# Kernel optimization log

Measured on AMD Instinct MI355X. Metric: run time of the kernel, lower is better.

Reference implementation:

```python
import jax, jax.numpy as jnp
import numpy as np

N = 50000
E = 600000
D = 128
EPS = 1e-5  # nn.LayerNorm default eps


def gcn_conv(x, W, b, src, dst):
    # PyG GCNConv with add_self_loops=True, edge_weight=None (all ones),
    # symmetric normalization D^-1/2 (A+I) D^-1/2.
    h = x @ W                                        # [N, D]
    deg = jnp.zeros((N,), h.dtype).at[dst].add(1.0) + 1.0  # +1 for self loop
    dinv = jax.lax.rsqrt(deg)                        # deg >= 1, safe
    norm = dinv[src] * dinv[dst]                     # [E]
    msg = h[src] * norm[:, None]                     # [E, D] gather
    agg = jax.ops.segment_sum(msg, dst, num_segments=N)
    agg = agg + h * (dinv * dinv)[:, None]           # self-loop term
    return agg + b


def layer_norm(x, g, b):
    mu = jnp.mean(x, axis=-1, keepdims=True)
    var = jnp.mean(jnp.square(x - mu), axis=-1, keepdims=True)
    return (x - mu) * jax.lax.rsqrt(var + EPS) * g + b


def setup_inputs() -> dict:
    key = jax.random.key(0)
    ks = jax.random.split(key, 6)
    x = jax.random.normal(ks[0], (N, D), dtype=jnp.float32)
    edge_index = jax.random.randint(ks[1], (2, E), 0, N, dtype=jnp.int64)
    s = 1.0 / np.sqrt(D)
    W1 = jax.random.uniform(ks[2], (D, D), jnp.float32, -s, s)
    W2 = jax.random.uniform(ks[3], (D, D), jnp.float32, -s, s)
    b1 = jnp.zeros((D,), jnp.float32)
    b2 = jnp.zeros((D,), jnp.float32)
    ln1_g = jnp.ones((D,), jnp.float32)
    ln1_b = jnp.zeros((D,), jnp.float32)
    ln2_g = jnp.ones((D,), jnp.float32)
    ln2_b = jnp.zeros((D,), jnp.float32)
    return {"x": x, "edge_index": edge_index, "W1": W1, "b1": b1,
            "ln1_g": ln1_g, "ln1_b": ln1_b, "W2": W2, "b2": b2,
            "ln2_g": ln2_g, "ln2_b": ln2_b}


def reference(x, edge_index, W1, b1, ln1_g, ln1_b, W2, b2, ln2_g, ln2_b):
    src, dst = edge_index[0], edge_index[1]
    out = gcn_conv(x, W1, b1, src, dst)
    out = jax.nn.relu(layer_norm(out, ln1_g, ln1_b))  # dropout = identity (eval)
    out = gcn_conv(out, W2, b2, src, dst)
    out = jax.nn.relu(layer_norm(out, ln2_g, ln2_b))
    return out + x
```

## Files before the change

kernel.cpp:

```cpp
#include <hip/hip_runtime.h>
#include <hip/hip_fp16.h>

#define D 128
#define EPS 1e-5f
#define KB 64
#define NBSH 7
#define BUCKW 128

typedef unsigned int u32;
typedef unsigned short u16;
typedef unsigned char u8;
typedef __attribute__((ext_vector_type(8))) _Float16 half8;
typedef __attribute__((ext_vector_type(4))) float f32x4;
typedef __attribute__((ext_vector_type(2))) float f32x2;

__device__ inline u16 f2h(float x) {
  _Float16 t = (_Float16)x;
  return __builtin_bit_cast(u16, t);
}
__device__ inline u8 f2fp8(float x) {
  return (u8)(__builtin_amdgcn_cvt_pk_fp8_f32(x, x, 0, false) & 0xff);
}

__global__ __launch_bounds__(256) void k_prep(const float* __restrict__ W1,
                                              const float* __restrict__ W2,
                                              u16* __restrict__ Wt1,
                                              u16* __restrict__ Wt2) {
  int i = blockIdx.x * 256 + threadIdx.x;
  if (i < 2 * D * D) {
    const float* W = (i < D * D) ? W1 : W2;
    u16* Wt = (i < D * D) ? Wt1 : Wt2;
    int ii = i & (D * D - 1);
    int k = ii >> 7, c = ii & 127;
    Wt[c * D + k] = f2h(W[ii]);
  }
}

template <bool F32IN>
__device__ __forceinline__ void gemm_body(const void* __restrict__ in_,
                                          const u16* __restrict__ Wt,
                                          u8* __restrict__ out, int nrows,
                                          int blk) {
  const int tid = threadIdx.x;
  const int lane = tid & 63, wv = tid >> 6;
  const int m = lane & 15, q = lane >> 4;
  const int r0 = blk * 64 + wv * 16;
  const int rowa = min(r0 + m, nrows - 1);

  f32x4 acc[8];
#pragma unroll
  for (int ct = 0; ct < 8; ct++) acc[ct] = (f32x4)(0.0f);

#pragma unroll
  for (int kk = 0; kk < 4; kk++) {
    const int kbase = kk * 32 + q * 8;
    half8 a;
    if (F32IN) {
      const float* in = (const float*)in_;
      float4 v0 = *(const float4*)(in + (size_t)rowa * D + kbase);
      float4 v1 = *(const float4*)(in + (size_t)rowa * D + kbase + 4);
      a[0] = (_Float16)v0.x; a[1] = (_Float16)v0.y;
      a[2] = (_Float16)v0.z; a[3] = (_Float16)v0.w;
      a[4] = (_Float16)v1.x; a[5] = (_Float16)v1.y;
      a[6] = (_Float16)v1.z; a[7] = (_Float16)v1.w;
    } else {
      const u16* in = (const u16*)in_;
      a = *(const half8*)(in + (size_t)rowa * D + kbase);
    }
#pragma unroll
    for (int ct = 0; ct < 8; ct++) {
      half8 b = *(const half8*)(Wt + (ct * 16 + m) * D + kbase);
      acc[ct] = __builtin_amdgcn_mfma_f32_16x16x32_f16(a, b, acc[ct], 0, 0, 0);
    }
  }

#pragma unroll
  for (int ct = 0; ct < 8; ct++) {
#pragma unroll
    for (int rg = 0; rg < 4; rg++) {
      int rr = r0 + q * 4 + rg;
      if (rr < nrows) out[(size_t)rr * D + ct * 16 + m] = f2fp8(acc[ct][rg]);
    }
  }
}

__global__ __launch_bounds__(256) void k_count_gemm1(
    const int* __restrict__ dst, int* __restrict__ cnt, int E, int NB, int EPB,
    const float* __restrict__ x, const u16* __restrict__ Wt1,
    u8* __restrict__ A, int nrows) {
  if (blockIdx.x < (u32)KB) {
    __shared__ int hist[512];
    const int k = blockIdx.x, tid = threadIdx.x;
    for (int i = tid; i < NB; i += 256) hist[i] = 0;
    __syncthreads();
    const int e0 = k * EPB, e1 = min(E, e0 + EPB);
    for (int base = e0 + tid; base < e1; base += 2048) {
      int dd[8];
#pragma unroll
      for (int i = 0; i < 8; i++) {
        int e = base + i * 256;
        dd[i] = (e < e1) ? dst[e] : -1;
      }
#pragma unroll
      for (int i = 0; i < 8; i++)
        if (dd[i] >= 0) atomicAdd(&hist[dd[i] >> NBSH], 1);
    }
    __syncthreads();
    for (int b = tid; b < NB; b += 256) cnt[b * KB + k] = hist[b];
  } else {
    gemm_body<true>(x, Wt1, A, nrows, blockIdx.x - KB);
  }
}

__global__ __launch_bounds__(1024) void k_scan(int* __restrict__ cnt, int M,
                                               int NB, int* __restrict__ bsv,
                                               int E) {
  __shared__ int wt[16];
  const int tid = threadIdx.x;
  const int lane = tid & 63, wid = tid >> 6;
  const int chunks = (M + 1023) >> 10;
  int running = 0;
  int i = tid;
  int v = (i < M) ? cnt[i] : 0;
  for (int c = 0; c < chunks; c++) {
    int inext = i + 1024;
    int vnext = (c + 1 < chunks && inext < M) ? cnt[inext] : 0;
    int incl = v;
#pragma unroll
    for (int o = 1; o < 64; o <<= 1) {
      int t = __shfl_up(incl, o, 64);
      if (lane >= o) incl += t;
    }
    if (lane == 63) wt[wid] = incl;
    __syncthreads();
    int woff = 0, total = 0;
#pragma unroll
    for (int j = 0; j < 16; j++) {
      int t = wt[j];
      if (j < wid) woff += t;
      total += t;
    }
    int excl = running + woff + incl - v;
    if (i < M) {
      cnt[i] = excl;
      if ((i & (KB - 1)) == 0) bsv[i / KB] = excl;
    }
    running += total;
    __syncthreads();
    i = inext;
    v = vnext;
  }
  if (tid == 0) bsv[NB] = E;
}

__global__ __launch_bounds__(256) void k_scatter(
    const int* __restrict__ src, const int* __restrict__ dst,
    const int* __restrict__ cnt, u32* __restrict__ tmp, int E, int NB,
    int EPB) {
  __shared__ int off[512];
  const int k = blockIdx.x, tid = threadIdx.x;
  for (int b = tid; b < NB; b += 256) off[b] = cnt[b * KB + k];
  __syncthreads();
  const int e0 = k * EPB, e1 = min(E, e0 + EPB);
  for (int base = e0 + tid; base < e1; base += 2048) {
    int dd[8], ss[8];
#pragma unroll
    for (int i = 0; i < 8; i++) {
      int e = base + i * 256;
      dd[i] = (e < e1) ? dst[e] : -1;
      ss[i] = (e < e1) ? src[e] : 0;
    }
#pragma unroll
    for (int i = 0; i < 8; i++) {
      if (dd[i] >= 0) {
        int p = atomicAdd(&off[dd[i] >> NBSH], 1);
        tmp[p] = (u32)ss[i] | ((u32)(dd[i] & (BUCKW - 1)) << 16);
      }
    }
  }
}

__global__ __launch_bounds__(256) void k_bucket(
    const u32* __restrict__ tmp, const int* __restrict__ bsv,
    int4* __restrict__ meta, float* __restrict__ dinv,
    u32* __restrict__ csr, int N) {
  __shared__ int hist[BUCKW];
  __shared__ int sc[BUCKW];
  __shared__ int cur[BUCKW];
  const int b = blockIdx.x, tid = threadIdx.x;
  const int s0 = bsv[b], s1 = bsv[b + 1];
  if (tid < BUCKW) hist[tid] = 0;
  __syncthreads();
  for (int base = s0 + tid; base < s1; base += 1024) {
    int tt[4];
#pragma unroll
    for (int i = 0; i < 4; i++) {
      int idx = base + i * 256;
      tt[i] = (idx < s1) ? (int)tmp[idx] : -1;
    }
#pragma unroll
    for (int i = 0; i < 4; i++)
      if (tt[i] >= 0) atomicAdd(&hist[(tt[i] >> 16) & (BUCKW - 1)], 1);
  }
  __syncthreads();
  if (tid < BUCKW) sc[tid] = hist[tid];
  __syncthreads();
#pragma unroll
  for (int o = 1; o < BUCKW; o <<= 1) {
    int t = 0;
    if (tid < BUCKW && tid >= o) t = sc[tid - o];
    __syncthreads();
    if (tid < BUCKW) sc[tid] += t;
    __syncthreads();
  }
  if (tid < BUCKW) {
    int dg = hist[tid];
    int excl = sc[tid] - dg;
    cur[tid] = excl;
    int d = (b << NBSH) + tid;
    if (d < N) {
      float dv = rsqrtf((float)dg + 1.0f);
      meta[d] = make_int4(s0 + excl, dg, __builtin_bit_cast(int, dv), 0);
      dinv[d] = dv;
    }
  }
  __syncthreads();
  for (int base = s0 + tid; base < s1; base += 1024) {
    int tt[4];
#pragma unroll
    for (int i = 0; i < 4; i++) {
      int idx = base + i * 256;
      tt[i] = (idx < s1) ? (int)tmp[idx] : -1;
    }
#pragma unroll
    for (int i = 0; i < 4; i++) {
      if (tt[i] >= 0) {
        int r = atomicAdd(&cur[(tt[i] >> 16) & (BUCKW - 1)], 1);
        csr[s0 + r] = (u32)tt[i] & 0xffffu;
      }
    }
  }
}

__global__ __launch_bounds__(256) void k_weights(
    const int4* __restrict__ meta, const float* __restrict__ dinv,
    u32* __restrict__ csr, int N) {
  int gid = blockIdx.x * 256 + threadIdx.x;
  int r = gid >> 2, j0 = gid & 3;
  if (r >= N) return;
  int4 mt = meta[r];
  float dv = __builtin_bit_cast(float, mt.z);
  for (int j = j0; j < mt.y; j += 4) {
    u32 s = csr[mt.x + j];
    float w = dinv[s] * dv;
    csr[mt.x + j] = s | ((u32)f2h(w) << 16);
  }
}

#define ACC_EDGE(vv, ee)                                                     \
  {                                                                          \
    float ww = (float)__builtin_bit_cast(_Float16, (u16)((ee) >> 16));       \
    f32x2 p_;                                                                \
    p_ = __builtin_amdgcn_cvt_pk_f32_fp8(vv.x, false);                       \
    acc[0] = fmaf(p_[0], ww, acc[0]); acc[1] = fmaf(p_[1], ww, acc[1]);      \
    p_ = __builtin_amdgcn_cvt_pk_f32_fp8(vv.x, true);                        \
    acc[2] = fmaf(p_[0], ww, acc[2]); acc[3] = fmaf(p_[1], ww, acc[3]);      \
    p_ = __builtin_amdgcn_cvt_pk_f32_fp8(vv.y, false);                       \
    acc[4] = fmaf(p_[0], ww, acc[4]); acc[5] = fmaf(p_[1], ww, acc[5]);      \
    p_ = __builtin_amdgcn_cvt_pk_f32_fp8(vv.y, true);                        \
    acc[6] = fmaf(p_[0], ww, acc[6]); acc[7] = fmaf(p_[1], ww, acc[7]);      \
  }

__device__ __forceinline__ void gather_ln_core(
    const uint2* __restrict__ hb, const int4* __restrict__ meta,
    const u32* __restrict__ csr, const float* __restrict__ b,
    const float* __restrict__ g, const float* __restrict__ bln,
    int row, int n, int sl, float out[8]) {
  const bool valid = row < n;
  const int rc = valid ? row : 0;
  int4 mt = meta[rc];
  int beg = mt.x;
  int cnt = valid ? mt.y : 0;
  float dv = __builtin_bit_cast(float, mt.z);
  float sn = dv * dv;

  float acc[8];
  {
    uint2 su = hb[(size_t)rc * 16 + sl];
    f32x2 p0 = __builtin_amdgcn_cvt_pk_f32_fp8(su.x, false);
    f32x2 p1 = __builtin_amdgcn_cvt_pk_f32_fp8(su.x, true);
    f32x2 p2 = __builtin_amdgcn_cvt_pk_f32_fp8(su.y, false);
    f32x2 p3 = __builtin_amdgcn_cvt_pk_f32_fp8(su.y, true);
    acc[0] = p0[0] * sn; acc[1] = p0[1] * sn;
    acc[2] = p1[0] * sn; acc[3] = p1[1] * sn;
    acc[4] = p2[0] * sn; acc[5] = p2[1] * sn;
    acc[6] = p3[0] * sn; acc[7] = p3[1] * sn;
  }

  int cm = max(cnt, __shfl_xor(cnt, 16, 64));
  cm = max(cm, __shfl_xor(cm, 32, 64));

  u32 epre = 0u;
  if (sl < cnt) epre = csr[beg + sl];

  for (int j0 = 0; j0 < cm; j0 += 16) {
    u32 ecur = epre;
    epre = 0u;
    {
      int nj = j0 + 16;
      if (nj < cm && sl < cnt - nj) epre = csr[beg + nj + sl];
    }
    int mm = min(cm - j0, 16);
    for (int j = 0; j < mm; j += 8) {
      u32 e0 = __shfl(ecur, j + 0, 16), e1 = __shfl(ecur, j + 1, 16);
      u32 e2 = __shfl(ecur, j + 2, 16), e3 = __shfl(ecur, j + 3, 16);
      u32 e4 = __shfl(ecur, j + 4, 16), e5 = __shfl(ecur, j + 5, 16);
      u32 e6 = __shfl(ecur, j + 6, 16), e7 = __shfl(ecur, j + 7, 16);
      uint2 v0 = hb[(size_t)(e0 & 0xffffu) * 16 + sl];
      uint2 v1 = hb[(size_t)(e1 & 0xffffu) * 16 + sl];
      uint2 v2 = hb[(size_t)(e2 & 0xffffu) * 16 + sl];
      uint2 v3 = hb[(size_t)(e3 & 0xffffu) * 16 + sl];
      uint2 v4 = hb[(size_t)(e4 & 0xffffu) * 16 + sl];
      uint2 v5 = hb[(size_t)(e5 & 0xffffu) * 16 + sl];
      uint2 v6 = hb[(size_t)(e6 & 0xffffu) * 16 + sl];
      uint2 v7 = hb[(size_t)(e7 & 0xffffu) * 16 + sl];
      ACC_EDGE(v0, e0);
      ACC_EDGE(v1, e1);
      ACC_EDGE(v2, e2);
      ACC_EDGE(v3, e3);
      ACC_EDGE(v4, e4);
      ACC_EDGE(v5, e5);
      ACC_EDGE(v6, e6);
      ACC_EDGE(v7, e7);
    }
  }

  int d0 = sl * 8;
  float4 bb0 = *(const float4*)(b + d0);
  float4 bb1 = *(const float4*)(b + d0 + 4);
  float a0 = acc[0] + bb0.x, a1 = acc[1] + bb0.y;
  float a2 = acc[2] + bb0.z, a3 = acc[3] + bb0.w;
  float a4 = acc[4] + bb1.x, a5 = acc[5] + bb1.y;
  float a6 = acc[6] + bb1.z, a7 = acc[7] + bb1.w;

  float sum = ((a0 + a1) + (a2 + a3)) + ((a4 + a5) + (a6 + a7));
#pragma unroll
  for (int o = 8; o >= 1; o >>= 1) sum += __shfl_xor(sum, o, 16);
  float mu = sum * (1.0f / 128.0f);
  float e0 = a0 - mu, e1 = a1 - mu, e2 = a2 - mu, e3 = a3 - mu;
  float e4 = a4 - mu, e5 = a5 - mu, e6 = a6 - mu, e7 = a7 - mu;
  float vs = ((e0 * e0 + e1 * e1) + (e2 * e2 + e3 * e3)) +
             ((e4 * e4 + e5 * e5) + (e6 * e6 + e7 * e7));
#pragma unroll
  for (int o = 8; o >= 1; o >>= 1) vs += __shfl_xor(vs, o, 16);
  float inv = rsqrtf(vs * (1.0f / 128.0f) + EPS);

  float4 gg0 = *(const float4*)(g + d0);
  float4 gg1 = *(const float4*)(g + d0 + 4);
  float4 bl0 = *(const float4*)(bln + d0);
  float4 bl1 = *(const float4*)(bln + d0 + 4);
  out[0] = fmaxf(e0 * inv * gg0.x + bl0.x, 0.0f);
  out[1] = fmaxf(e1 * inv * gg0.y + bl0.y, 0.0f);
  out[2] = fmaxf(e2 * inv * gg0.z + bl0.z, 0.0f);
  out[3] = fmaxf(e3 * inv * gg0.w + bl0.w, 0.0f);
  out[4] = fmaxf(e4 * inv * gg1.x + bl1.x, 0.0f);
  out[5] = fmaxf(e5 * inv * gg1.y + bl1.y, 0.0f);
  out[6] = fmaxf(e6 * inv * gg1.z + bl1.z, 0.0f);
  out[7] = fmaxf(e7 * inv * gg1.w + bl1.w, 0.0f);
}

__global__ __launch_bounds__(256, 8) void k_gather1(
    const uint2* __restrict__ hb, const int4* __restrict__ meta,
    const u32* __restrict__ csr,
    const float* __restrict__ b, const float* __restrict__ g,
    const float* __restrict__ bln,
    u16* __restrict__ y1, int n) {
  const int tid = threadIdx.x;
  const int sl = tid & 15;
  const int row = blockIdx.x * 16 + (tid >> 4);
  float o[8];
  gather_ln_core(hb, meta, csr, b, g, bln, row, n, sl, o);
  if (row >= n) return;
  uint4 pk;
  pk.x = ((u32)f2h(o[1]) << 16) | (u32)f2h(o[0]);
  pk.y = ((u32)f2h(o[3]) << 16) | (u32)f2h(o[2]);
  pk.z = ((u32)f2h(o[5]) << 16) | (u32)f2h(o[4]);
  pk.w = ((u32)f2h(o[7]) << 16) | (u32)f2h(o[6]);
  *(uint4*)(y1 + (size_t)row * D + sl * 8) = pk;
}

__global__ __launch_bounds__(256) void k_gemm2(const u16* __restrict__ y1,
                                               const u16* __restrict__ Wt2,
                                               u8* __restrict__ outB, int n) {
  gemm_body<false>(y1, Wt2, outB, n, blockIdx.x);
}

__global__ __launch_bounds__(256, 8) void k_gather2(
    const uint2* __restrict__ hb, const int4* __restrict__ meta,
    const u32* __restrict__ csr,
    const float* __restrict__ b, const float* __restrict__ g,
    const float* __restrict__ bln, const float* __restrict__ resid,
    float* __restrict__ outf, int n) {
  const int tid = threadIdx.x;
  const int sl = tid & 15;
  const int row = blockIdx.x * 16 + (tid >> 4);
  float o[8];
  gather_ln_core(hb, meta, csr, b, g, bln, row, n, sl, o);
  if (row >= n) return;
  size_t base = (size_t)row * D + sl * 8;
  float4 r0 = *(const float4*)(resid + base);
  float4 r1 = *(const float4*)(resid + base + 4);
  *(float4*)(outf + base) =
      make_float4(o[0] + r0.x, o[1] + r0.y, o[2] + r0.z, o[3] + r0.w);
  *(float4*)(outf + base + 4) =
      make_float4(o[4] + r1.x, o[5] + r1.y, o[6] + r1.z, o[7] + r1.w);
}

extern "C" void kernel_launch(void* const* d_in, const int* in_sizes, int n_in,
                              void* d_out, int out_size, void* d_ws, size_t ws_size,
                              hipStream_t stream) {
  const float* x    = (const float*)d_in[0];
  const int*   ei   = (const int*)d_in[1];
  const float* W1   = (const float*)d_in[2];
  const float* b1   = (const float*)d_in[3];
  const float* g1   = (const float*)d_in[4];
  const float* bl1  = (const float*)d_in[5];
  const float* W2   = (const float*)d_in[6];
  const float* b2   = (const float*)d_in[7];
  const float* g2   = (const float*)d_in[8];
  const float* bl2  = (const float*)d_in[9];

  const int N = in_sizes[0] / D;
  const int E = in_sizes[1] / 2;
  const int* src = ei;
  const int* dst = ei + E;

  const int NB  = (N + BUCKW - 1) / BUCKW;
  const int M   = NB * KB;
  const int EPB = (E + KB - 1) / KB;
  const int GB  = (N + 63) / 64;
  const int RB  = (N + 15) / 16;

  size_t off = 0;
  auto walloc = [&](size_t bytes) {
    void* p = (char*)d_ws + off;
    off = (off + bytes + 255) & ~(size_t)255;
    return p;
  };
  int*   cnt   = (int*)walloc((size_t)M * 4);
  int*   bsv   = (int*)walloc((size_t)(NB + 1) * 4);
  u32*   tmp   = (u32*)walloc((size_t)E * 4);
  u32*   csr   = (u32*)walloc((size_t)E * 4);
  int4*  meta  = (int4*)walloc((size_t)N * 16);
  float* dinv  = (float*)walloc((size_t)N * 4);
  u8*    A     = (u8*)walloc((size_t)N * D);
  u8*    B     = (u8*)walloc((size_t)N * D);
  u16*   Wt1   = (u16*)walloc((size_t)D * D * 2);
  u16*   Wt2   = (u16*)walloc((size_t)D * D * 2);
  u16*   y1    = (u16*)walloc((size_t)N * D * 2);
  float* O     = (float*)d_out;

  k_prep<<<(2 * D * D + 255) / 256, 256, 0, stream>>>(W1, W2, Wt1, Wt2);
  k_count_gemm1<<<KB + GB, 256, 0, stream>>>(dst, cnt, E, NB, EPB, x, Wt1, A, N);
  k_scan<<<1, 1024, 0, stream>>>(cnt, M, NB, bsv, E);
  k_scatter<<<KB, 256, 0, stream>>>(src, dst, cnt, tmp, E, NB, EPB);
  k_bucket<<<NB, 256, 0, stream>>>(tmp, bsv, meta, dinv, csr, N);
  k_weights<<<(N * 4 + 255) / 256, 256, 0, stream>>>(meta, dinv, csr, N);
  k_gather1<<<RB, 256, 0, stream>>>((const uint2*)A, meta, csr, b1, g1, bl1,
                                    y1, N);
  k_gemm2<<<GB, 256, 0, stream>>>(y1, Wt2, B, N);
  k_gather2<<<RB, 256, 0, stream>>>((const uint2*)B, meta, csr,
                                    b2, g2, bl2, x, O, N);
}
```

Before: 207.8 us.

## Build CSR via global per-node degree atomics instead of bucketed two-level sort

Replaces the bucketed counting sort (per-block histograms, scan, scatter, per-bucket local sort, separate weight pass) with per-node global atomic degree counts, a single scan over N nodes that also writes meta and dinv, and one scatter that places edges with their normalization weights already packed. This removes three kernel launches and the temporary edge buffer. It relies on global atomics to contended addresses and a single-block scan over 50k entries. The CSR order within a row becomes nondeterministic, which can change fp summation order. The gather loop also drops the shuffle-based prefetch of edge indices and loads them directly per lane instead.

```diff
diff --git a/kernel.cpp b/kernel.cpp
--- a/kernel.cpp
+++ b/kernel.cpp
@@ -3,9 +3,7 @@
 
 #define D 128
 #define EPS 1e-5f
-#define KB 64
-#define NBSH 7
-#define BUCKW 128
+#define CB 128
 
 typedef unsigned int u32;
 typedef unsigned short u16;
@@ -25,14 +23,18 @@
 __global__ __launch_bounds__(256) void k_prep(const float* __restrict__ W1,
                                               const float* __restrict__ W2,
                                               u16* __restrict__ Wt1,
-                                              u16* __restrict__ Wt2) {
-  int i = blockIdx.x * 256 + threadIdx.x;
-  if (i < 2 * D * D) {
+                                              u16* __restrict__ Wt2,
+                                              int* __restrict__ deg, int N) {
+  if (blockIdx.x < 128) {
+    int i = blockIdx.x * 256 + threadIdx.x;
     const float* W = (i < D * D) ? W1 : W2;
     u16* Wt = (i < D * D) ? Wt1 : Wt2;
     int ii = i & (D * D - 1);
     int k = ii >> 7, c = ii & 127;
     Wt[c * D + k] = f2h(W[ii]);
+  } else {
+    int i = (blockIdx.x - 128) * 256 + threadIdx.x;
+    if (i < N) deg[i] = 0;
   }
 }
 
@@ -85,46 +87,43 @@
 }
 
 __global__ __launch_bounds__(256) void k_count_gemm1(
-    const int* __restrict__ dst, int* __restrict__ cnt, int E, int NB, int EPB,
+    const int* __restrict__ dst, int* __restrict__ deg, int E, int EPB,
     const float* __restrict__ x, const u16* __restrict__ Wt1,
     u8* __restrict__ A, int nrows) {
-  if (blockIdx.x < (u32)KB) {
-    __shared__ int hist[512];
+  if (blockIdx.x < (u32)CB) {
     const int k = blockIdx.x, tid = threadIdx.x;
-    for (int i = tid; i < NB; i += 256) hist[i] = 0;
-    __syncthreads();
     const int e0 = k * EPB, e1 = min(E, e0 + EPB);
-    for (int base = e0 + tid; base < e1; base += 2048) {
-      int dd[8];
-#pragma unroll
-      for (int i = 0; i < 8; i++) {
+    for (int base = e0 + tid; base < e1; base += 1024) {
+      int dd[4];
+#pragma unroll
+      for (int i = 0; i < 4; i++) {
         int e = base + i * 256;
         dd[i] = (e < e1) ? dst[e] : -1;
       }
 #pragma unroll
-      for (int i = 0; i < 8; i++)
-        if (dd[i] >= 0) atomicAdd(&hist[dd[i] >> NBSH], 1);
-    }
-    __syncthreads();
-    for (int b = tid; b < NB; b += 256) cnt[b * KB + k] = hist[b];
+      for (int i = 0; i < 4; i++)
+        if (dd[i] >= 0) atomicAdd(&deg[dd[i]], 1);
+    }
   } else {
-    gemm_body<true>(x, Wt1, A, nrows, blockIdx.x - KB);
-  }
-}
-
-__global__ __launch_bounds__(1024) void k_scan(int* __restrict__ cnt, int M,
-                                               int NB, int* __restrict__ bsv,
-                                               int E) {
+    gemm_body<true>(x, Wt1, A, nrows, blockIdx.x - CB);
+  }
+}
+
+__global__ __launch_bounds__(1024) void k_scan(const int* __restrict__ deg,
+                                               int4* __restrict__ meta,
+                                               float* __restrict__ dinv,
+                                               int* __restrict__ cursor,
+                                               int N) {
   __shared__ int wt[16];
   const int tid = threadIdx.x;
   const int lane = tid & 63, wid = tid >> 6;
-  const int chunks = (M + 1023) >> 10;
+  const int chunks = (N + 1023) >> 10;
   int running = 0;
   int i = tid;
-  int v = (i < M) ? cnt[i] : 0;
+  int v = (i < N) ? deg[i] : 0;
   for (int c = 0; c < chunks; c++) {
     int inext = i + 1024;
-    int vnext = (c + 1 < chunks && inext < M) ? cnt[inext] : 0;
+    int vnext = (c + 1 < chunks && inext < N) ? deg[inext] : 0;
     int incl = v;
 #pragma unroll
     for (int o = 1; o < 64; o <<= 1) {
@@ -141,119 +140,46 @@
       total += t;
     }
     int excl = running + woff + incl - v;
-    if (i < M) {
-      cnt[i] = excl;
-      if ((i & (KB - 1)) == 0) bsv[i / KB] = excl;
+    if (i < N) {
+      float dv = rsqrtf((float)v + 1.0f);
+      meta[i] = make_int4(excl, v, __builtin_bit_cast(int, dv), 0);
+      dinv[i] = dv;
+      cursor[i] = excl;
     }
     running += total;
     __syncthreads();
     i = inext;
     v = vnext;
   }
-  if (tid == 0) bsv[NB] = E;
-}
-
-__global__ __launch_bounds__(256) void k_scatter(
+}
+
+__global__ __launch_bounds__(256) void k_scatter2(
     const int* __restrict__ src, const int* __restrict__ dst,
-    const int* __restrict__ cnt, u32* __restrict__ tmp, int E, int NB,
-    int EPB) {
-  __shared__ int off[512];
-  const int k = blockIdx.x, tid = threadIdx.x;
-  for (int b = tid; b < NB; b += 256) off[b] = cnt[b * KB + k];
-  __syncthreads();
-  const int e0 = k * EPB, e1 = min(E, e0 + EPB);
-  for (int base = e0 + tid; base < e1; base += 2048) {
-    int dd[8], ss[8];
-#pragma unroll
-    for (int i = 0; i < 8; i++) {
-      int e = base + i * 256;
-      dd[i] = (e < e1) ? dst[e] : -1;
-      ss[i] = (e < e1) ? src[e] : 0;
-    }
-#pragma unroll
-    for (int i = 0; i < 8; i++) {
+    const float* __restrict__ dinv, int* __restrict__ cursor,
+    u32* __restrict__ csr, int E) {
+  const int stride = gridDim.x * 256;
+  int gid = blockIdx.x * 256 + threadIdx.x;
+  for (int base = gid; base < E; base += stride * 4) {
+    int ss[4], dd[4];
+#pragma unroll
+    for (int i = 0; i < 4; i++) {
+      int e = base + i * stride;
+      ss[i] = (e < E) ? src[e] : 0;
+      dd[i] = (e < E) ? dst[e] : -1;
+    }
+    float ws[4], wd[4];
+#pragma unroll
+    for (int i = 0; i < 4; i++) {
+      ws[i] = (dd[i] >= 0) ? dinv[ss[i]] : 0.0f;
+      wd[i] = (dd[i] >= 0) ? dinv[dd[i]] : 0.0f;
+    }
+#pragma unroll
+    for (int i = 0; i < 4; i++) {
       if (dd[i] >= 0) {
-        int p = atomicAdd(&off[dd[i] >> NBSH], 1);
-        tmp[p] = (u32)ss[i] | ((u32)(dd[i] & (BUCKW - 1)) << 16);
+        int p = atomicAdd(&cursor[dd[i]], 1);
+        csr[p] = (u32)ss[i] | ((u32)f2h(ws[i] * wd[i]) << 16);
       }
     }
-  }
-}
-
-__global__ __launch_bounds__(256) void k_bucket(
-    const u32* __restrict__ tmp, const int* __restrict__ bsv,
-    int4* __restrict__ meta, float* __restrict__ dinv,
-    u32* __restrict__ csr, int N) {
-  __shared__ int hist[BUCKW];
-  __shared__ int sc[BUCKW];
-  __shared__ int cur[BUCKW];
-  const int b = blockIdx.x, tid = threadIdx.x;
-  const int s0 = bsv[b], s1 = bsv[b + 1];
-  if (tid < BUCKW) hist[tid] = 0;
-  __syncthreads();
-  for (int base = s0 + tid; base < s1; base += 1024) {
-    int tt[4];
-#pragma unroll
-    for (int i = 0; i < 4; i++) {
-      int idx = base + i * 256;
-      tt[i] = (idx < s1) ? (int)tmp[idx] : -1;
-    }
-#pragma unroll
-    for (int i = 0; i < 4; i++)
-      if (tt[i] >= 0) atomicAdd(&hist[(tt[i] >> 16) & (BUCKW - 1)], 1);
-  }
-  __syncthreads();
-  if (tid < BUCKW) sc[tid] = hist[tid];
-  __syncthreads();
-#pragma unroll
-  for (int o = 1; o < BUCKW; o <<= 1) {
-    int t = 0;
-    if (tid < BUCKW && tid >= o) t = sc[tid - o];
-    __syncthreads();
-    if (tid < BUCKW) sc[tid] += t;
-    __syncthreads();
-  }
-  if (tid < BUCKW) {
-    int dg = hist[tid];
-    int excl = sc[tid] - dg;
-    cur[tid] = excl;
-    int d = (b << NBSH) + tid;
-    if (d < N) {
-      float dv = rsqrtf((float)dg + 1.0f);
-      meta[d] = make_int4(s0 + excl, dg, __builtin_bit_cast(int, dv), 0);
-      dinv[d] = dv;
-    }
-  }
-  __syncthreads();
-  for (int base = s0 + tid; base < s1; base += 1024) {
-    int tt[4];
-#pragma unroll
-    for (int i = 0; i < 4; i++) {
-      int idx = base + i * 256;
-      tt[i] = (idx < s1) ? (int)tmp[idx] : -1;
-    }
-#pragma unroll
-    for (int i = 0; i < 4; i++) {
-      if (tt[i] >= 0) {
-        int r = atomicAdd(&cur[(tt[i] >> 16) & (BUCKW - 1)], 1);
-        csr[s0 + r] = (u32)tt[i] & 0xffffu;
-      }
-    }
-  }
-}
-
-__global__ __launch_bounds__(256) void k_weights(
-    const int4* __restrict__ meta, const float* __restrict__ dinv,
-    u32* __restrict__ csr, int N) {
-  int gid = blockIdx.x * 256 + threadIdx.x;
-  int r = gid >> 2, j0 = gid & 3;
-  if (r >= N) return;
-  int4 mt = meta[r];
-  float dv = __builtin_bit_cast(float, mt.z);
-  for (int j = j0; j < mt.y; j += 4) {
-    u32 s = csr[mt.x + j];
-    float w = dinv[s] * dv;
-    csr[mt.x + j] = s | ((u32)f2h(w) << 16);
   }
 }
 
@@ -300,39 +226,19 @@
   int cm = max(cnt, __shfl_xor(cnt, 16, 64));
   cm = max(cm, __shfl_xor(cm, 32, 64));
 
-  u32 epre = 0u;
-  if (sl < cnt) epre = csr[beg + sl];
-
-  for (int j0 = 0; j0 < cm; j0 += 16) {
-    u32 ecur = epre;
-    epre = 0u;
-    {
-      int nj = j0 + 16;
-      if (nj < cm && sl < cnt - nj) epre = csr[beg + nj + sl];
-    }
-    int mm = min(cm - j0, 16);
-    for (int j = 0; j < mm; j += 8) {
-      u32 e0 = __shfl(ecur, j + 0, 16), e1 = __shfl(ecur, j + 1, 16);
-      u32 e2 = __shfl(ecur, j + 2, 16), e3 = __shfl(ecur, j + 3, 16);
-      u32 e4 = __shfl(ecur, j + 4, 16), e5 = __shfl(ecur, j + 5, 16);
-      u32 e6 = __shfl(ecur, j + 6, 16), e7 = __shfl(ecur, j + 7, 16);
-      uint2 v0 = hb[(size_t)(e0 & 0xffffu) * 16 + sl];
-      uint2 v1 = hb[(size_t)(e1 & 0xffffu) * 16 + sl];
-      uint2 v2 = hb[(size_t)(e2 & 0xffffu) * 16 + sl];
-      uint2 v3 = hb[(size_t)(e3 & 0xffffu) * 16 + sl];
-      uint2 v4 = hb[(size_t)(e4 & 0xffffu) * 16 + sl];
-      uint2 v5 = hb[(size_t)(e5 & 0xffffu) * 16 + sl];
-      uint2 v6 = hb[(size_t)(e6 & 0xffffu) * 16 + sl];
-      uint2 v7 = hb[(size_t)(e7 & 0xffffu) * 16 + sl];
-      ACC_EDGE(v0, e0);
-      ACC_EDGE(v1, e1);
-      ACC_EDGE(v2, e2);
-      ACC_EDGE(v3, e3);
-      ACC_EDGE(v4, e4);
-      ACC_EDGE(v5, e5);
-      ACC_EDGE(v6, e6);
-      ACC_EDGE(v7, e7);
-    }
+  for (int j0 = 0; j0 < cm; j0 += 8) {
+    u32 e[8];
+#pragma unroll
+    for (int jj = 0; jj < 8; jj++) {
+      int j = j0 + jj;
+      e[jj] = (j < cnt) ? csr[beg + j] : 0u;
+    }
+    uint2 v[8];
+#pragma unroll
+    for (int jj = 0; jj < 8; jj++)
+      v[jj] = hb[(size_t)(e[jj] & 0xffffu) * 16 + sl];
+#pragma unroll
+    for (int jj = 0; jj < 8; jj++) ACC_EDGE(v[jj], e[jj]);
   }
 
   int d0 = sl * 8;
@@ -435,11 +341,10 @@
   const int* src = ei;
   const int* dst = ei + E;
 
-  const int NB  = (N + BUCKW - 1) / BUCKW;
-  const int M   = NB * KB;
-  const int EPB = (E + KB - 1) / KB;
+  const int EPB = (E + CB - 1) / CB;
   const int GB  = (N + 63) / 64;
   const int RB  = (N + 15) / 16;
+  const int ZB  = (N + 255) / 256;
 
   size_t off = 0;
   auto walloc = [&](size_t bytes) {
@@ -447,10 +352,9 @@
     off = (off + bytes + 255) & ~(size_t)255;
     return p;
   };
-  int*   cnt   = (int*)walloc((size_t)M * 4);
-  int*   bsv   = (int*)walloc((size_t)(NB + 1) * 4);
-  u32*   tmp   = (u32*)walloc((size_t)E * 4);
-  u32*   csr   = (u32*)walloc((size_t)E * 4);
+  int*   deg   = (int*)walloc((size_t)N * 4);
+  int*   cursor= (int*)walloc((size_t)N * 4);
+  u32*   csr   = (u32*)walloc((size_t)E * 4 + 256);
   int4*  meta  = (int4*)walloc((size_t)N * 16);
   float* dinv  = (float*)walloc((size_t)N * 4);
   u8*    A     = (u8*)walloc((size_t)N * D);
@@ -460,12 +364,10 @@
   u16*   y1    = (u16*)walloc((size_t)N * D * 2);
   float* O     = (float*)d_out;
 
-  k_prep<<<(2 * D * D + 255) / 256, 256, 0, stream>>>(W1, W2, Wt1, Wt2);
-  k_count_gemm1<<<KB + GB, 256, 0, stream>>>(dst, cnt, E, NB, EPB, x, Wt1, A, N);
-  k_scan<<<1, 1024, 0, stream>>>(cnt, M, NB, bsv, E);
-  k_scatter<<<KB, 256, 0, stream>>>(src, dst, cnt, tmp, E, NB, EPB);
-  k_bucket<<<NB, 256, 0, stream>>>(tmp, bsv, meta, dinv, csr, N);
-  k_weights<<<(N * 4 + 255) / 256, 256, 0, stream>>>(meta, dinv, csr, N);
+  k_prep<<<128 + ZB, 256, 0, stream>>>(W1, W2, Wt1, Wt2, deg, N);
+  k_count_gemm1<<<CB + GB, 256, 0, stream>>>(dst, deg, E, EPB, x, Wt1, A, N);
+  k_scan<<<1, 1024, 0, stream>>>(deg, meta, dinv, cursor, N);
+  k_scatter2<<<512, 256, 0, stream>>>(src, dst, dinv, cursor, csr, E);
   k_gather1<<<RB, 256, 0, stream>>>((const uint2*)A, meta, csr, b1, g1, bl1,
                                     y1, N);
   k_gemm2<<<GB, 256, 0, stream>>>(y1, Wt2, B, N);
```

Result: slower. 272.1 us (+30.9%).

## Parallelize prefix scan across blocks and simplify gather edge-loading loop

Applied to the files above, without the earlier changes.

Replaces the single-block 1024-thread scan over the bucket count matrix with a three-kernel reduce/mid-scan/apply scheme that spreads the work over many blocks. The scan over M=NB*64 (~25k) entries was serialized in one workgroup. Separately, the gather loop drops the shuffle-based prefetch of CSR entries and instead has each lane load 8 CSR entries directly (broadcast loads) before issuing 8 feature gathers. This adds two extra kernel launches and loses the explicit next-chunk prefetch.

```diff
diff --git a/kernel.cpp b/kernel.cpp
--- a/kernel.cpp
+++ b/kernel.cpp
@@ -112,45 +112,86 @@
   }
 }
 
-__global__ __launch_bounds__(1024) void k_scan(int* __restrict__ cnt, int M,
-                                               int NB, int* __restrict__ bsv,
-                                               int E) {
-  __shared__ int wt[16];
-  const int tid = threadIdx.x;
-  const int lane = tid & 63, wid = tid >> 6;
-  const int chunks = (M + 1023) >> 10;
+__global__ __launch_bounds__(256) void k_scan_reduce(
+    const int* __restrict__ cnt, int M, int* __restrict__ bsum) {
+  const int b = blockIdx.x, t = threadIdx.x;
+  const int lane = t & 63, w = t >> 6;
+  int idx = b * 1024 + t * 4;
+  int4 v = make_int4(0, 0, 0, 0);
+  if (idx + 3 < M) {
+    v = *(const int4*)(cnt + idx);
+  } else {
+    if (idx + 0 < M) v.x = cnt[idx + 0];
+    if (idx + 1 < M) v.y = cnt[idx + 1];
+    if (idx + 2 < M) v.z = cnt[idx + 2];
+  }
+  int s = v.x + v.y + v.z + v.w;
+#pragma unroll
+  for (int o = 1; o < 64; o <<= 1) s += __shfl_xor(s, o, 64);
+  __shared__ int ws[4];
+  if (lane == 0) ws[w] = s;
+  __syncthreads();
+  if (t == 0) bsum[b] = ws[0] + ws[1] + ws[2] + ws[3];
+}
+
+__global__ __launch_bounds__(64) void k_scan_mid(const int* __restrict__ bsum,
+                                                 int* __restrict__ boff,
+                                                 int SB, int* __restrict__ bsv,
+                                                 int NB, int E) {
+  const int lane = threadIdx.x;
   int running = 0;
-  int i = tid;
-  int v = (i < M) ? cnt[i] : 0;
-  for (int c = 0; c < chunks; c++) {
-    int inext = i + 1024;
-    int vnext = (c + 1 < chunks && inext < M) ? cnt[inext] : 0;
+  for (int base = 0; base < SB; base += 64) {
+    int i = base + lane;
+    int v = (i < SB) ? bsum[i] : 0;
     int incl = v;
 #pragma unroll
     for (int o = 1; o < 64; o <<= 1) {
       int t = __shfl_up(incl, o, 64);
       if (lane >= o) incl += t;
     }
-    if (lane == 63) wt[wid] = incl;
-    __syncthreads();
-    int woff = 0, total = 0;
-#pragma unroll
-    for (int j = 0; j < 16; j++) {
-      int t = wt[j];
-      if (j < wid) woff += t;
-      total += t;
-    }
-    int excl = running + woff + incl - v;
-    if (i < M) {
-      cnt[i] = excl;
-      if ((i & (KB - 1)) == 0) bsv[i / KB] = excl;
-    }
-    running += total;
-    __syncthreads();
-    i = inext;
-    v = vnext;
-  }
-  if (tid == 0) bsv[NB] = E;
+    if (i < SB) boff[i] = running + incl - v;
+    running += __shfl(incl, 63, 64);
+  }
+  if (lane == 0) bsv[NB] = E;
+}
+
+__global__ __launch_bounds__(256) void k_scan_apply(
+    int* __restrict__ cnt, int M, const int* __restrict__ boff,
+    int* __restrict__ bsv) {
+  const int b = blockIdx.x, t = threadIdx.x;
+  const int lane = t & 63, w = t >> 6;
+  int idx = b * 1024 + t * 4;
+  int4 v = make_int4(0, 0, 0, 0);
+  if (idx + 3 < M) {
+    v = *(const int4*)(cnt + idx);
+  } else {
+    if (idx + 0 < M) v.x = cnt[idx + 0];
+    if (idx + 1 < M) v.y = cnt[idx + 1];
+    if (idx + 2 < M) v.z = cnt[idx + 2];
+  }
+  int s = v.x + v.y + v.z + v.w;
+  int incl = s;
+#pragma unroll
+  for (int o = 1; o < 64; o <<= 1) {
+    int u = __shfl_up(incl, o, 64);
+    if (lane >= o) incl += u;
+  }
+  __shared__ int ws[4];
+  if (lane == 63) ws[w] = incl;
+  __syncthreads();
+  int wbase = 0;
+#pragma unroll
+  for (int j = 0; j < 4; j++)
+    if (j < w) wbase += ws[j];
+  int base = boff[b] + wbase + incl - s;
+  int e0 = base, e1 = e0 + v.x, e2 = e1 + v.y, e3 = e2 + v.z;
+  if (idx < M) {
+    cnt[idx] = e0;
+    if ((idx & (KB - 1)) == 0) bsv[idx >> 6] = e0;
+  }
+  if (idx + 1 < M) cnt[idx + 1] = e1;
+  if (idx + 2 < M) cnt[idx + 2] = e2;
+  if (idx + 3 < M) cnt[idx + 3] = e3;
 }
 
 __global__ __launch_bounds__(256) void k_scatter(
@@ -300,39 +341,19 @@
   int cm = max(cnt, __shfl_xor(cnt, 16, 64));
   cm = max(cm, __shfl_xor(cm, 32, 64));
 
-  u32 epre = 0u;
-  if (sl < cnt) epre = csr[beg + sl];
-
-  for (int j0 = 0; j0 < cm; j0 += 16) {
-    u32 ecur = epre;
-    epre = 0u;
-    {
-      int nj = j0 + 16;
-      if (nj < cm && sl < cnt - nj) epre = csr[beg + nj + sl];
-    }
-    int mm = min(cm - j0, 16);
-    for (int j = 0; j < mm; j += 8) {
-      u32 e0 = __shfl(ecur, j + 0, 16), e1 = __shfl(ecur, j + 1, 16);
-      u32 e2 = __shfl(ecur, j + 2, 16), e3 = __shfl(ecur, j + 3, 16);
-      u32 e4 = __shfl(ecur, j + 4, 16), e5 = __shfl(ecur, j + 5, 16);
-      u32 e6 = __shfl(ecur, j + 6, 16), e7 = __shfl(ecur, j + 7, 16);
-      uint2 v0 = hb[(size_t)(e0 & 0xffffu) * 16 + sl];
-      uint2 v1 = hb[(size_t)(e1 & 0xffffu) * 16 + sl];
-      uint2 v2 = hb[(size_t)(e2 & 0xffffu) * 16 + sl];
-      uint2 v3 = hb[(size_t)(e3 & 0xffffu) * 16 + sl];
-      uint2 v4 = hb[(size_t)(e4 & 0xffffu) * 16 + sl];
-      uint2 v5 = hb[(size_t)(e5 & 0xffffu) * 16 + sl];
-      uint2 v6 = hb[(size_t)(e6 & 0xffffu) * 16 + sl];
-      uint2 v7 = hb[(size_t)(e7 & 0xffffu) * 16 + sl];
-      ACC_EDGE(v0, e0);
-      ACC_EDGE(v1, e1);
-      ACC_EDGE(v2, e2);
-      ACC_EDGE(v3, e3);
-      ACC_EDGE(v4, e4);
-      ACC_EDGE(v5, e5);
-      ACC_EDGE(v6, e6);
-      ACC_EDGE(v7, e7);
-    }
+  for (int j0 = 0; j0 < cm; j0 += 8) {
+    u32 e[8];
+#pragma unroll
+    for (int jj = 0; jj < 8; jj++) {
+      int j = j0 + jj;
+      e[jj] = (j < cnt) ? csr[beg + j] : 0u;
+    }
+    uint2 v[8];
+#pragma unroll
+    for (int jj = 0; jj < 8; jj++)
+      v[jj] = hb[(size_t)(e[jj] & 0xffffu) * 16 + sl];
+#pragma unroll
+    for (int jj = 0; jj < 8; jj++) ACC_EDGE(v[jj], e[jj]);
   }
 
   int d0 = sl * 8;
@@ -440,6 +461,7 @@
   const int EPB = (E + KB - 1) / KB;
   const int GB  = (N + 63) / 64;
   const int RB  = (N + 15) / 16;
+  const int SB  = (M + 1023) / 1024;
 
   size_t off = 0;
   auto walloc = [&](size_t bytes) {
@@ -448,6 +470,8 @@
     return p;
   };
   int*   cnt   = (int*)walloc((size_t)M * 4);
+  int*   bsum  = (int*)walloc((size_t)SB * 4);
+  int*   boff  = (int*)walloc((size_t)SB * 4);
   int*   bsv   = (int*)walloc((size_t)(NB + 1) * 4);
   u32*   tmp   = (u32*)walloc((size_t)E * 4);
   u32*   csr   = (u32*)walloc((size_t)E * 4);
@@ -462,7 +486,9 @@
 
   k_prep<<<(2 * D * D + 255) / 256, 256, 0, stream>>>(W1, W2, Wt1, Wt2);
   k_count_gemm1<<<KB + GB, 256, 0, stream>>>(dst, cnt, E, NB, EPB, x, Wt1, A, N);
-  k_scan<<<1, 1024, 0, stream>>>(cnt, M, NB, bsv, E);
+  k_scan_reduce<<<SB, 256, 0, stream>>>(cnt, M, bsum);
+  k_scan_mid<<<1, 64, 0, stream>>>(bsum, boff, SB, bsv, NB, E);
+  k_scan_apply<<<SB, 256, 0, stream>>>(cnt, M, boff, bsv);
   k_scatter<<<KB, 256, 0, stream>>>(src, dst, cnt, tmp, E, NB, EPB);
   k_bucket<<<NB, 256, 0, stream>>>(tmp, bsv, meta, dinv, csr, N);
   k_weights<<<(N * 4 + 255) / 256, 256, 0, stream>>>(meta, dinv, csr, N);
```

Result: faster. 193.8 us (-6.7%).
